# Performance work log

Hardware: AMD Instinct MI355X
Metric: run time of the kernel (lower is better)

Reference implementation:

```python
import jax, jax.numpy as jnp
import numpy as np

H = 512

def setup_inputs() -> dict:
    key = jax.random.key(0)
    k1, k2, k3, k4 = jax.random.split(key, 4)
    B, S_dec, S_enc = 8, 2048, 2048
    encoder_output = jax.random.normal(k1, (B, S_enc, H), dtype=jnp.float32)
    decoder_output = jax.random.normal(k2, (B, S_dec, H), dtype=jnp.float32)
    # nn.Bilinear(H, H, 1): weight [1, H, H], bias [1]; init U(-1/sqrt(H), 1/sqrt(H))
    bound = 1.0 / np.sqrt(H)
    W = jax.random.uniform(k3, (1, H, H), dtype=jnp.float32, minval=-bound, maxval=bound)
    b = jax.random.uniform(k4, (1,), dtype=jnp.float32, minval=-bound, maxval=bound)
    return {"encoder_output": encoder_output, "decoder_output": decoder_output, "W": W, "b": b}

def reference(encoder_output, decoder_output, W, b):
    # Original: scores[b,d,e] = Bilinear(enc[b,e], dec[b,d]) = enc[b,e] @ W[0] @ dec[b,d] + bias
    # Computed as two GEMMs instead of expanding to [B, S_dec, S_enc, H].
    encW = jnp.einsum('beh,hg->beg', encoder_output, W[0])   # [B, S_enc, H]
    scores = jnp.einsum('beg,bdg->bde', encW, decoder_output) + b[0]  # [B, S_dec, S_enc]
    return scores
```

## Files before the change

### kernel.cpp

```cpp
#include <hip/hip_runtime.h>

typedef __attribute__((ext_vector_type(8))) short short8;
typedef __attribute__((ext_vector_type(4))) float f32x4;
typedef __attribute__((ext_vector_type(8))) unsigned short ushort8;

__device__ __forceinline__ unsigned short f2bf(float x) {
  union { float f; unsigned u; } v; v.f = x;
  unsigned r = v.u + 0x7fffu + ((v.u >> 16) & 1u);
  return (unsigned short)(r >> 16);
}

__global__ __launch_bounds__(256) void wt_kernel(
    const float* __restrict__ W, unsigned short* __restrict__ Wt) {
  __shared__ float s[64][65];
  int g0 = blockIdx.x * 64, h0 = blockIdx.y * 64;
  int tx = threadIdx.x & 63, ty = threadIdx.x >> 6;
#pragma unroll
  for (int rr = 0; rr < 16; ++rr) {
    int h = ty * 16 + rr;
    s[h][tx] = W[(long)(h0 + h) * 512 + g0 + tx];
  }
  __syncthreads();
#pragma unroll
  for (int rr = 0; rr < 16; ++rr) {
    int g = ty * 16 + rr;
    Wt[(long)(g0 + g) * 512 + h0 + tx] = f2bf(s[tx][g]);
  }
}

__global__ __launch_bounds__(256) void gemm1_plus_cvtdec(
    const float* __restrict__ enc, const unsigned short* __restrict__ Wt,
    unsigned short* __restrict__ encW,
    const float* __restrict__ dec, unsigned short* __restrict__ dec_bf) {
  if (blockIdx.x >= 512) {
    int i = (blockIdx.x - 512) * 256 + threadIdx.x;
    const float4* p = (const float4*)(dec + (long)i * 8);
    float4 a = p[0], b = p[1];
    ushort8 o;
    o[0] = f2bf(a.x); o[1] = f2bf(a.y); o[2] = f2bf(a.z); o[3] = f2bf(a.w);
    o[4] = f2bf(b.x); o[5] = f2bf(b.y); o[6] = f2bf(b.z); o[7] = f2bf(b.w);
    *(ushort8*)(dec_bf + (long)i * 8) = o;
    return;
  }

  constexpr int K = 512, N = 512, BK = 32;
  __shared__ __align__(16) short As[128 * BK];
  __shared__ __align__(16) short Bs[128 * BK];

  const int g = blockIdx.x;
  const int work = (g & 7) * 64 + (g >> 3);
  const int bxm = work >> 2, byn = work & 3;

  const int tid = threadIdx.x;
  const int wave = tid >> 6, lane = tid & 63;
  const int wm = wave >> 1, wn = wave & 1;
  const int r = lane & 15, q = lane >> 4;

  const float* Ab = enc + (long)bxm * 128 * K;
  const unsigned short* Bb = Wt + (long)byn * 128 * K;

  const int srow = tid >> 1, shalf = tid & 1;
  const float* arow = Ab + (long)srow * K + shalf * 16;

  f32x4 acc[4][4] = {};
  float4 av[4];
#pragma unroll
  for (int j = 0; j < 4; ++j) av[j] = ((const float4*)arow)[j];

  for (int kt = 0; kt < K; kt += BK) {
    ushort8 o0, o1;
    o0[0] = f2bf(av[0].x); o0[1] = f2bf(av[0].y); o0[2] = f2bf(av[0].z); o0[3] = f2bf(av[0].w);
    o0[4] = f2bf(av[1].x); o0[5] = f2bf(av[1].y); o0[6] = f2bf(av[1].z); o0[7] = f2bf(av[1].w);
    o1[0] = f2bf(av[2].x); o1[1] = f2bf(av[2].y); o1[2] = f2bf(av[2].z); o1[3] = f2bf(av[2].w);
    o1[4] = f2bf(av[3].x); o1[5] = f2bf(av[3].y); o1[6] = f2bf(av[3].z); o1[7] = f2bf(av[3].w);
    *(ushort8*)&As[srow * BK + shalf * 16 + 0] = o0;
    *(ushort8*)&As[srow * BK + shalf * 16 + 8] = o1;

#pragma unroll
    for (int j = 0; j < 2; ++j) {
      int c = (j * 4 + wave) * 64 + lane;
      int row = c >> 2;
      int coff = (c & 3) * 8;
      __builtin_amdgcn_global_load_lds(
          (const __attribute__((address_space(1))) void*)(Bb + (long)row * K + kt + coff),
          (__attribute__((address_space(3))) void*)(Bs + (j * 4 + wave) * 512),
          16, 0, 0);
    }
    __syncthreads();

    short8 af[4], bfr[4];
#pragma unroll
    for (int m = 0; m < 4; ++m)
      af[m] = *(const short8*)&As[(wm * 64 + m * 16 + r) * BK + q * 8];
#pragma unroll
    for (int n = 0; n < 4; ++n)
      bfr[n] = *(const short8*)&Bs[(wn * 64 + n * 16 + r) * BK + q * 8];

    if (kt + BK < K) {
      const float* ap = arow + kt + BK;
#pragma unroll
      for (int j = 0; j < 4; ++j) av[j] = ((const float4*)ap)[j];
    }

#pragma unroll
    for (int m = 0; m < 4; ++m)
#pragma unroll
      for (int n = 0; n < 4; ++n)
        acc[m][n] = __builtin_amdgcn_mfma_f32_16x16x32_bf16(af[m], bfr[n], acc[m][n], 0, 0, 0);
    __syncthreads();
  }

  const long rowbase = (long)bxm * 128 + wm * 64;
  const long colbase = (long)byn * 128 + wn * 64;
#pragma unroll
  for (int m = 0; m < 4; ++m)
#pragma unroll
    for (int n = 0; n < 4; ++n)
#pragma unroll
      for (int j = 0; j < 4; ++j) {
        long row = rowbase + m * 16 + q * 4 + j;
        long col = colbase + n * 16 + r;
        encW[row * (long)N + col] = f2bf(acc[m][n][j]);
      }
}


#define VMCNT(n) asm volatile("s_waitcnt vmcnt(" #n ")" ::: "memory")

#define STAGE(GP, LBASE, tt, kkv)                                             \
  do {                                                                        \
    _Pragma("unroll") for (int j_ = 0; j_ < 2; ++j_) {                        \
      int c_ = w * 2 + j_;                                                    \
      __builtin_amdgcn_global_load_lds(                                       \
          (const __attribute__((address_space(1))) void*)(                    \
              (GP) + ((long)(c_ * 16 + srow)) * 512 + (tt) * 64 + (kkv) * 32 + scol), \
          (__attribute__((address_space(3))) void*)((LBASE) + (c_ << 10)),    \
          16, 0, 0);                                                          \
    }                                                                         \
  } while (0)

#define PHASE(Ac, Bc, kkv, mb, LOADB, STAGE_STMT, ENDWAIT_STMT)               \
  do {                                                                        \
    if (LOADB) {                                                              \
      _Pragma("unroll") for (int n_ = 0; n_ < 4; ++n_)                        \
        bf[kkv][n_] = *(const short8*)((Bc) + (kkv) * 16384 +                 \
                                       ((wn * 4 + n_) << 10) + lconst);       \
    }                                                                         \
    _Pragma("unroll") for (int i_ = 0; i_ < 4; ++i_)                          \
      af[i_] = *(const short8*)((Ac) + (kkv) * 16384 +                        \
                                ((wm * 8 + (mb) + i_) << 10) + lconst);       \
    STAGE_STMT;                                                               \
    __builtin_amdgcn_s_barrier();                                             \
    asm volatile("s_waitcnt lgkmcnt(0)" ::: "memory");                        \
    __builtin_amdgcn_sched_barrier(0);                                        \
    __builtin_amdgcn_s_setprio(1);                                            \
    _Pragma("unroll") for (int i_ = 0; i_ < 4; ++i_)                          \
      _Pragma("unroll") for (int n_ = 0; n_ < 4; ++n_)                        \
        acc[(mb) + i_][n_] = __builtin_amdgcn_mfma_f32_16x16x32_bf16(         \
            af[i_], bf[kkv][n_], acc[(mb) + i_][n_], 0, 0, 0);                \
    __builtin_amdgcn_s_setprio(0);                                            \
    ENDWAIT_STMT;                                                             \
    __builtin_amdgcn_s_barrier();                                             \
  } while (0)

__global__ __launch_bounds__(512, 2) void gemm2_8ph(
    const unsigned short* __restrict__ A,
    const unsigned short* __restrict__ Bt,
    float* __restrict__ C, const float* __restrict__ bias) {
  __shared__ __align__(16) char Lds[131072];
#define LDS_A(d) (Lds + (d) * 32768)
#define LDS_B(d) (Lds + 65536 + (d) * 32768)

  int flat = blockIdx.x;
  int sw = (flat & 7) * 64 + (flat >> 3);
  int z = sw >> 6, xy = sw & 63, bx = xy & 7, by = xy >> 3;

  const int tid = threadIdx.x;
  const int w = tid >> 6, lane = tid & 63;
  const int wm = w >> 2, wn = w & 3;
  const int base_r = lane & 15, q = lane >> 4;
  const int lconst = base_r * 64 + ((q * 16) ^ ((base_r & 8) << 2));
  const int srow = lane >> 2;
  const int scol = ((lane & 3) * 8) ^ (((lane >> 5) & 1) << 4);

  const unsigned short* Ab = A + ((long)z * 2048 + bx * 256) * 512;
  const unsigned short* Bb = Bt + ((long)z * 2048 + by * 256) * 512;

  f32x4 acc[8][4] = {};
  short8 af[4];
  short8 bf[2][4];

  STAGE(Ab, LDS_A(0), 0, 0);
  STAGE(Bb, LDS_B(0), 0, 0);
  STAGE(Ab, LDS_A(0) + 16384, 0, 1);
  STAGE(Bb, LDS_B(0) + 16384, 0, 1);
  VMCNT(4);
  __builtin_amdgcn_s_barrier();

  for (int t = 0; t < 7; ++t) {
    const char* Ac = LDS_A(t & 1);
    const char* Bc = LDS_B(t & 1);
    char* An = LDS_A((t + 1) & 1);
    char* Bn = LDS_B((t + 1) & 1);
    PHASE(Ac, Bc, 0, 0, true,  STAGE(Ab, An, t + 1, 0),         (void)0);
    PHASE(Ac, Bc, 0, 4, false, STAGE(Bb, Bn, t + 1, 0),         VMCNT(4));
    PHASE(Ac, Bc, 1, 0, true,  STAGE(Ab, An + 16384, t + 1, 1), (void)0);
    PHASE(Ac, Bc, 1, 4, false, STAGE(Bb, Bn + 16384, t + 1, 1), VMCNT(4));
  }
  {
    const char* Ac = LDS_A(1);
    const char* Bc = LDS_B(1);
    PHASE(Ac, Bc, 0, 0, true,  (void)0, (void)0);
    PHASE(Ac, Bc, 0, 4, false, (void)0, VMCNT(0));
    PHASE(Ac, Bc, 1, 0, true,  (void)0, (void)0);
    PHASE(Ac, Bc, 1, 4, false, (void)0, (void)0);
  }

  const float bv = bias[0];
  float* Cb = C + ((long)z * 2048 + bx * 256 + wm * 128) * 2048 + by * 256 + wn * 64;
#pragma unroll
  for (int m = 0; m < 8; ++m)
#pragma unroll
    for (int n = 0; n < 4; ++n)
#pragma unroll
      for (int j = 0; j < 4; ++j)
        Cb[(long)(m * 16 + q * 4 + j) * 2048 + n * 16 + base_r] = acc[m][n][j] + bv;
#undef LDS_A
#undef LDS_B
}

extern "C" void kernel_launch(void* const* d_in, const int* in_sizes, int n_in,
                              void* d_out, int out_size, void* d_ws, size_t ws_size,
                              hipStream_t stream) {
  const float* enc  = (const float*)d_in[0];
  const float* dec  = (const float*)d_in[1];
  const float* W    = (const float*)d_in[2];
  const float* bias = (const float*)d_in[3];
  float* out = (float*)d_out;

  constexpr int Bn = 8, S = 2048, H = 512;
  constexpr long NE = (long)Bn * S * H;

  unsigned short* dec_bf = (unsigned short*)d_ws;
  unsigned short* Wt     = dec_bf + NE;
  unsigned short* encW   = Wt + (long)H * H;

  wt_kernel<<<dim3(8, 8), 256, 0, stream>>>(W, Wt);

  gemm1_plus_cvtdec<<<dim3(512 + 4096, 1, 1), 256, 0, stream>>>(
      enc, Wt, encW, dec, dec_bf);

  gemm2_8ph<<<dim3(512, 1, 1), 512, 0, stream>>>(dec_bf, encW, out, bias);
}
```

Baseline: 83.47 us.

## Replace 8-phase 256x256 GEMM2 with simple 128x128 single-buffered kernel

Swaps the hand-pipelined 256x256-tile, 512-thread, double-buffered second GEMM for a plain 128x128-tile, 256-thread kernel with a single LDS buffer. Each K step loads once, syncs, then issues MFMAs, with no overlap or LDS swizzle. The smaller tiles and LDS footprint allow four blocks per CU and a 2048-block grid. In exchange, loads no longer overlap compute, operands get less reuse, and unswizzled LDS reads may hit bank conflicts.

```diff
diff --git a/kernel.cpp b/kernel.cpp
--- a/kernel.cpp
+++ b/kernel.cpp
@@ -124,109 +124,70 @@
       }
 }
 
-
-#define VMCNT(n) asm volatile("s_waitcnt vmcnt(" #n ")" ::: "memory")
-
-#define STAGE(GP, LBASE, tt, kkv)                                             \
-  do {                                                                        \
-    _Pragma("unroll") for (int j_ = 0; j_ < 2; ++j_) {                        \
-      int c_ = w * 2 + j_;                                                    \
-      __builtin_amdgcn_global_load_lds(                                       \
-          (const __attribute__((address_space(1))) void*)(                    \
-              (GP) + ((long)(c_ * 16 + srow)) * 512 + (tt) * 64 + (kkv) * 32 + scol), \
-          (__attribute__((address_space(3))) void*)((LBASE) + (c_ << 10)),    \
-          16, 0, 0);                                                          \
-    }                                                                         \
-  } while (0)
-
-#define PHASE(Ac, Bc, kkv, mb, LOADB, STAGE_STMT, ENDWAIT_STMT)               \
-  do {                                                                        \
-    if (LOADB) {                                                              \
-      _Pragma("unroll") for (int n_ = 0; n_ < 4; ++n_)                        \
-        bf[kkv][n_] = *(const short8*)((Bc) + (kkv) * 16384 +                 \
-                                       ((wn * 4 + n_) << 10) + lconst);       \
-    }                                                                         \
-    _Pragma("unroll") for (int i_ = 0; i_ < 4; ++i_)                          \
-      af[i_] = *(const short8*)((Ac) + (kkv) * 16384 +                        \
-                                ((wm * 8 + (mb) + i_) << 10) + lconst);       \
-    STAGE_STMT;                                                               \
-    __builtin_amdgcn_s_barrier();                                             \
-    asm volatile("s_waitcnt lgkmcnt(0)" ::: "memory");                        \
-    __builtin_amdgcn_sched_barrier(0);                                        \
-    __builtin_amdgcn_s_setprio(1);                                            \
-    _Pragma("unroll") for (int i_ = 0; i_ < 4; ++i_)                          \
-      _Pragma("unroll") for (int n_ = 0; n_ < 4; ++n_)                        \
-        acc[(mb) + i_][n_] = __builtin_amdgcn_mfma_f32_16x16x32_bf16(         \
-            af[i_], bf[kkv][n_], acc[(mb) + i_][n_], 0, 0, 0);                \
-    __builtin_amdgcn_s_setprio(0);                                            \
-    ENDWAIT_STMT;                                                             \
-    __builtin_amdgcn_s_barrier();                                             \
-  } while (0)
-
-__global__ __launch_bounds__(512, 2) void gemm2_8ph(
+__global__ __launch_bounds__(256, 4) void gemm2_m97(
     const unsigned short* __restrict__ A,
     const unsigned short* __restrict__ Bt,
     float* __restrict__ C, const float* __restrict__ bias) {
-  __shared__ __align__(16) char Lds[131072];
-#define LDS_A(d) (Lds + (d) * 32768)
-#define LDS_B(d) (Lds + 65536 + (d) * 32768)
+  constexpr int K = 512, BK = 32;
+  __shared__ __align__(16) short As[128 * BK];
+  __shared__ __align__(16) short Bs[128 * BK];
 
   int flat = blockIdx.x;
-  int sw = (flat & 7) * 64 + (flat >> 3);
-  int z = sw >> 6, xy = sw & 63, bx = xy & 7, by = xy >> 3;
+  int sw = (flat & 7) * 256 + (flat >> 3);
+  int z = sw >> 8, bx = (sw >> 4) & 15, by = sw & 15;
 
   const int tid = threadIdx.x;
-  const int w = tid >> 6, lane = tid & 63;
-  const int wm = w >> 2, wn = w & 3;
-  const int base_r = lane & 15, q = lane >> 4;
-  const int lconst = base_r * 64 + ((q * 16) ^ ((base_r & 8) << 2));
-  const int srow = lane >> 2;
-  const int scol = ((lane & 3) * 8) ^ (((lane >> 5) & 1) << 4);
-
-  const unsigned short* Ab = A + ((long)z * 2048 + bx * 256) * 512;
-  const unsigned short* Bb = Bt + ((long)z * 2048 + by * 256) * 512;
-
-  f32x4 acc[8][4] = {};
-  short8 af[4];
-  short8 bf[2][4];
-
-  STAGE(Ab, LDS_A(0), 0, 0);
-  STAGE(Bb, LDS_B(0), 0, 0);
-  STAGE(Ab, LDS_A(0) + 16384, 0, 1);
-  STAGE(Bb, LDS_B(0) + 16384, 0, 1);
-  VMCNT(4);
-  __builtin_amdgcn_s_barrier();
-
-  for (int t = 0; t < 7; ++t) {
-    const char* Ac = LDS_A(t & 1);
-    const char* Bc = LDS_B(t & 1);
-    char* An = LDS_A((t + 1) & 1);
-    char* Bn = LDS_B((t + 1) & 1);
-    PHASE(Ac, Bc, 0, 0, true,  STAGE(Ab, An, t + 1, 0),         (void)0);
-    PHASE(Ac, Bc, 0, 4, false, STAGE(Bb, Bn, t + 1, 0),         VMCNT(4));
-    PHASE(Ac, Bc, 1, 0, true,  STAGE(Ab, An + 16384, t + 1, 1), (void)0);
-    PHASE(Ac, Bc, 1, 4, false, STAGE(Bb, Bn + 16384, t + 1, 1), VMCNT(4));
-  }
-  {
-    const char* Ac = LDS_A(1);
-    const char* Bc = LDS_B(1);
-    PHASE(Ac, Bc, 0, 0, true,  (void)0, (void)0);
-    PHASE(Ac, Bc, 0, 4, false, (void)0, VMCNT(0));
-    PHASE(Ac, Bc, 1, 0, true,  (void)0, (void)0);
-    PHASE(Ac, Bc, 1, 4, false, (void)0, (void)0);
+  const int wave = tid >> 6, lane = tid & 63;
+  const int wm = wave >> 1, wn = wave & 1;
+  const int r = lane & 15, q = lane >> 4;
+
+  const unsigned short* Ab = A + ((long)z * 2048 + bx * 128) * 512;
+  const unsigned short* Bb = Bt + ((long)z * 2048 + by * 128) * 512;
+
+  f32x4 acc[4][4] = {};
+
+  for (int kt = 0; kt < K; kt += BK) {
+#pragma unroll
+    for (int j = 0; j < 2; ++j) {
+      int c = (j * 4 + wave) * 64 + lane;
+      int row = c >> 2;
+      int coff = (c & 3) * 8;
+      __builtin_amdgcn_global_load_lds(
+          (const __attribute__((address_space(1))) void*)(Ab + (long)row * K + kt + coff),
+          (__attribute__((address_space(3))) void*)(As + (j * 4 + wave) * 512),
+          16, 0, 0);
+      __builtin_amdgcn_global_load_lds(
+          (const __attribute__((address_space(1))) void*)(Bb + (long)row * K + kt + coff),
+          (__attribute__((address_space(3))) void*)(Bs + (j * 4 + wave) * 512),
+          16, 0, 0);
+    }
+    __syncthreads();
+
+    short8 af[4], bfr[4];
+#pragma unroll
+    for (int m = 0; m < 4; ++m)
+      af[m] = *(const short8*)&As[(wm * 64 + m * 16 + r) * BK + q * 8];
+#pragma unroll
+    for (int n = 0; n < 4; ++n)
+      bfr[n] = *(const short8*)&Bs[(wn * 64 + n * 16 + r) * BK + q * 8];
+
+#pragma unroll
+    for (int m = 0; m < 4; ++m)
+#pragma unroll
+      for (int n = 0; n < 4; ++n)
+        acc[m][n] = __builtin_amdgcn_mfma_f32_16x16x32_bf16(af[m], bfr[n], acc[m][n], 0, 0, 0);
+    __syncthreads();
   }
 
   const float bv = bias[0];
-  float* Cb = C + ((long)z * 2048 + bx * 256 + wm * 128) * 2048 + by * 256 + wn * 64;
-#pragma unroll
-  for (int m = 0; m < 8; ++m)
+  float* Cb = C + ((long)z * 2048 + bx * 128 + wm * 64) * 2048 + by * 128 + wn * 64;
+#pragma unroll
+  for (int m = 0; m < 4; ++m)
 #pragma unroll
     for (int n = 0; n < 4; ++n)
 #pragma unroll
       for (int j = 0; j < 4; ++j)
-        Cb[(long)(m * 16 + q * 4 + j) * 2048 + n * 16 + base_r] = acc[m][n][j] + bv;
-#undef LDS_A
-#undef LDS_B
+        Cb[(long)(m * 16 + q * 4 + j) * 2048 + n * 16 + r] = acc[m][n][j] + bv;
 }
 
 extern "C" void kernel_launch(void* const* d_in, const int* in_sizes, int n_in,
@@ -250,5 +211,5 @@
   gemm1_plus_cvtdec<<<dim3(512 + 4096, 1, 1), 256, 0, stream>>>(
       enc, Wt, encW, dec, dec_bf);
 
-  gemm2_8ph<<<dim3(512, 1, 1), 512, 0, stream>>>(dec_bf, encW, out, bias);
-}
+  gemm2_m97<<<dim3(2048, 1, 1), 256, 0, stream>>>(dec_bf, encW, out, bias);
+}
```

New measurement: 83.25 us. No clear change (-0.3%).
